# Optimization experiments

Measured on AMD Instinct MI355X. Metric: run time of the kernel, lower is better.

The kernel has to match this reference:

```python
import jax, jax.numpy as jnp
import numpy as np

DIM = 768
HEADS = 8

def setup_inputs() -> dict:
    key = jax.random.key(0)
    k1, k2, k3, k4 = jax.random.split(key, 4)
    x = jax.random.normal(k1, (4, 2048, DIM), dtype=jnp.float32)
    # torch Linear(D, 3D, bias=False): weight [3D, D]; store transposed [D, 3D]
    W_qkv = jax.random.normal(k2, (DIM, 3 * DIM), dtype=jnp.float32) * (DIM ** -0.5)
    W_o = jax.random.normal(k3, (DIM, DIM), dtype=jnp.float32) * (DIM ** -0.5)
    b_o = jax.random.normal(k4, (DIM,), dtype=jnp.float32) * 0.01
    return {"x": x, "W_qkv": W_qkv, "W_o": W_o, "b_o": b_o}

def reference(x, W_qkv, W_o, b_o):
    B, N, D = x.shape
    H = HEADS
    dh = D // H
    scale = dh ** -0.5
    qkv = x @ W_qkv                                   # [B, N, 3D]
    qkv = qkv.reshape(B, N, 3, H, dh)
    qkv = jnp.transpose(qkv, (2, 0, 3, 1, 4))         # [3, B, H, N, dh]
    Q, K, V = qkv[0], qkv[1], qkv[2]
    scores = jnp.einsum('bhqd,bhkd->bhqk', Q, K) * scale  # [B, H, N, N]
    attn = jax.nn.softmax(scores, axis=-1)
    out = jnp.einsum('bhqk,bhkd->bhqd', attn, V)      # [B, H, N, dh]
    # Faithful to original: reshape [B,H,N,dh] -> [B,N,D] WITHOUT head transpose
    out = out.reshape(B, N, D)
    return out @ W_o + b_o
```

## Files before the change

### kernel.cpp

```cpp
#include <hip/hip_runtime.h>

typedef __attribute__((ext_vector_type(8))) short short8;
typedef __attribute__((ext_vector_type(4))) float f32x4;
typedef __attribute__((ext_vector_type(4))) _Float16 half4;
typedef __attribute__((ext_vector_type(8))) _Float16 half8;
typedef __attribute__((ext_vector_type(2))) __fp16 fp16x2;

#define B_SZ 4
#define NSEQ 2048
#define DIM  768
#define NH   8
#define DH   96

__device__ __forceinline__ unsigned short f2bf(float f) {
  unsigned int u = __float_as_uint(f);
  u += 0x7fffu + ((u >> 16) & 1u);
  return (unsigned short)(u >> 16);
}

__device__ __forceinline__ float fexp2(float x) {
#if __has_builtin(__builtin_amdgcn_exp2f)
  return __builtin_amdgcn_exp2f(x);
#else
  return exp2f(x);
#endif
}

__device__ __forceinline__ void glds16(const void* g, void* l) {
  __builtin_amdgcn_global_load_lds((const __attribute__((address_space(1))) void*)g,
                                   (__attribute__((address_space(3))) void*)l, 16, 0, 0);
}

__global__ __launch_bounds__(256) void prep_kernel(
    const float* __restrict__ x, unsigned short* __restrict__ xb,
    const float* __restrict__ Wqkv, unsigned short* __restrict__ wqkvT,
    const float* __restrict__ Wo, unsigned short* __restrict__ woT)
{
  int blk = blockIdx.x;
  if (blk < 6144) {
    int i = blk * 256 + threadIdx.x;
    float4 v = ((const float4*)x)[i];
    ushort4 o;
    o.x = f2bf(v.x); o.y = f2bf(v.y); o.z = f2bf(v.z); o.w = f2bf(v.w);
    ((ushort4*)xb)[i] = o;
    return;
  }
  __shared__ float tile[32][33];
  const float* W; unsigned short* WT; int ncols, bx, by;
  if (blk < 7872) { int r = blk - 6144; W = Wqkv; WT = wqkvT; ncols = 2304; bx = r % 72; by = r / 72; }
  else            { int r = blk - 7872; W = Wo;   WT = woT;   ncols = 768;  bx = r % 24; by = r / 24; }
  int tx = threadIdx.x & 31, ty = threadIdx.x >> 5;
  int c0 = bx * 32, r0 = by * 32;
#pragma unroll
  for (int i = 0; i < 4; i++)
    tile[ty + i * 8][tx] = W[(size_t)(r0 + ty + i * 8) * ncols + c0 + tx];
  __syncthreads();
#pragma unroll
  for (int i = 0; i < 4; i++)
    WT[(size_t)(c0 + ty + i * 8) * 768 + r0 + tx] = f2bf(tile[tx][ty + i * 8]);
}

template <int EPI>
__global__ __launch_bounds__(256) void gemm_bt(
    const unsigned short* __restrict__ A, const unsigned short* __restrict__ Bt,
    unsigned short* __restrict__ qo, unsigned short* __restrict__ ko,
    _Float16* __restrict__ vo, float* __restrict__ fo,
    const float* __restrict__ bias)
{
  __shared__ unsigned short As[128 * 64];
  __shared__ unsigned short Bs[128 * 64];
  const int t = threadIdx.x;
  const int w = t >> 6, lane = t & 63;
  const int l15 = lane & 15, qd = lane >> 4;
  const int rsw = l15 & 7;
  const int m0 = blockIdx.y * 128, n0 = blockIdx.x * 128;
  const int wm = (w >> 1) * 64, wn = (w & 1) * 64;

  int off[2];
#pragma unroll
  for (int j = 0; j < 2; j++) {
    int cl = j * 64 + lane;
    int r16 = cl >> 3, c = cl & 7;
    off[j] = r16 * DIM + ((c ^ (r16 & 7)) * 8);
  }
  const unsigned short* ga = A  + (size_t)(m0 + w * 16) * DIM;
  const unsigned short* gb = Bt + (size_t)(n0 + w * 16) * DIM;

  f32x4 acc[4][4] = {};

  for (int k0 = 0; k0 < DIM; k0 += 64) {
#pragma unroll
    for (int j = 0; j < 2; j++) {
      glds16(ga + k0 + off[j],            &As[w * 1024 + j * 512]);
      glds16(ga + 64 * DIM + k0 + off[j], &As[4096 + w * 1024 + j * 512]);
      glds16(gb + k0 + off[j],            &Bs[w * 1024 + j * 512]);
      glds16(gb + 64 * DIM + k0 + off[j], &Bs[4096 + w * 1024 + j * 512]);
    }
    __syncthreads();
#pragma unroll
    for (int ks = 0; ks < 2; ks++) {
      short8 af[4], bfr[4];
#pragma unroll
      for (int i = 0; i < 4; i++)
        af[i]  = *(const short8*)&As[(wm + i * 16 + l15) * 64 + (((ks * 4 + qd) ^ rsw)) * 8];
#pragma unroll
      for (int i = 0; i < 4; i++)
        bfr[i] = *(const short8*)&Bs[(wn + i * 16 + l15) * 64 + (((ks * 4 + qd) ^ rsw)) * 8];
#pragma unroll
      for (int mi = 0; mi < 4; mi++)
#pragma unroll
        for (int ni = 0; ni < 4; ni++)
          acc[mi][ni] = __builtin_amdgcn_mfma_f32_16x16x32_bf16(af[mi], bfr[ni], acc[mi][ni], 0, 0, 0);
    }
    __syncthreads();
  }

#pragma unroll
  for (int mi = 0; mi < 4; mi++)
#pragma unroll
    for (int ni = 0; ni < 4; ni++) {
      int rowb = m0 + wm + mi * 16 + qd * 4;
      int col  = n0 + wn + ni * 16 + l15;
      if (EPI == 0) {
        int b = rowb >> 11, n = rowb & 2047;
        int s = col / DIM;
        int rem = col - s * DIM;
        int hh = rem / DH;
        int c = rem - hh * DH;
        size_t bh = (size_t)(b * NH + hh);
        if (s == 2) {
          half4 pk;
#pragma unroll
          for (int r = 0; r < 4; r++) pk[r] = (_Float16)acc[mi][ni][r];
          *(half4*)&vo[(bh * DH + c) * NSEQ + n] = pk;
        } else if (s == 0) {
#pragma unroll
          for (int r = 0; r < 4; r++)
            qo[(bh * NSEQ + n + r) * DH + c] = f2bf(acc[mi][ni][r] * 0.1472444679f);
        } else {
#pragma unroll
          for (int r = 0; r < 4; r++)
            ko[(bh * NSEQ + n + r) * DH + c] = f2bf(acc[mi][ni][r]);
        }
      } else {
#pragma unroll
        for (int r = 0; r < 4; r++)
          fo[(size_t)(rowb + r) * DIM + col] = acc[mi][ni][r] + bias[col];
      }
    }
}

__global__ __launch_bounds__(256, 2) void flash_kernel(
    const unsigned short* __restrict__ Qb, const unsigned short* __restrict__ Kb,
    const _Float16* __restrict__ Vtb, unsigned short* __restrict__ Z)
{
  __shared__ unsigned char smem[49152];

  const int t = threadIdx.x, w = t >> 6, lane = t & 63;
  const int l15 = lane & 15, qd = lane >> 4;
  const int swz = (l15 >> 1) & 3;
  const int vswz = l15 & 7;

  const int bid = blockIdx.x;
  const int h  = bid & 7;
  const int qt = (bid >> 3) & 15;
  const int b  = bid >> 7;

  const size_t bh = (size_t)(b * NH + h);
  const unsigned short* Qg = Qb + (bh * NSEQ + (size_t)qt * 128) * DH;
  const unsigned short* Kg = Kb + bh * NSEQ * DH;
  const _Float16*       Vg = Vtb + bh * (size_t)DH * NSEQ;

  int qoff[6];
#pragma unroll
  for (int i = 0; i < 6; i++) {
    int L = i * 256 + t;
    int r = L / 12, c = L - r * 12;
    qoff[i] = r * 96 + ((c ^ ((r >> 1) & 3)) * 8);
  }
  int koff[3];
#pragma unroll
  for (int i = 0; i < 3; i++) {
    int L = w * 192 + i * 64 + lane;
    int r = L / 12, c = L - r * 12;
    int fk = r >> 4, m = r & 15;
    int key = 32 * (fk & 1) + 4 * (fk >> 1) + 8 * (m >> 2) + (m & 3);
    koff[i] = key * 96 + ((c ^ ((r >> 1) & 3)) * 8);
  }
  int voff[3];
#pragma unroll
  for (int i = 0; i < 3; i++) {
    int L = i * 256 + t;
    int r = L >> 3, c = L & 7;
    voff[i] = r * NSEQ + ((c ^ (r & 7)) * 8);
  }

  short8 qa[2][3];
  f32x4 o[2][7] = {};
  const half8 onef = {(_Float16)1.f, (_Float16)1.f, (_Float16)1.f, (_Float16)1.f,
                      (_Float16)1.f, (_Float16)1.f, (_Float16)1.f, (_Float16)1.f};

  auto stK = [&](int j, int bufoff) {
    unsigned short* Kd = (unsigned short*)(smem + bufoff);
    const unsigned short* Kt = Kg + (size_t)j * 64 * DH;
#pragma unroll
    for (int i = 0; i < 3; i++)
      glds16(Kt + koff[i], &Kd[w * 1536 + i * 512]);
  };
  auto stV = [&](int j, int bufoff) {
    _Float16* Vd = (_Float16*)(smem + bufoff + 12288);
    const _Float16* Vt = Vg + j * 64;
#pragma unroll
    for (int i = 0; i < 3; i++)
      glds16(Vt + voff[i], &Vd[(i * 256 + w * 64) * 8]);
  };

#pragma unroll
  for (int i = 0; i < 6; i++)
    glds16(Qg + qoff[i], &((unsigned short*)(smem + 24576))[i * 2048 + w * 512]);
  stK(0, 0);
  stV(0, 0);
  __syncthreads();

  const unsigned short* Qs = (const unsigned short*)(smem + 24576);
#pragma unroll
  for (int fq = 0; fq < 2; fq++)
#pragma unroll
    for (int ks = 0; ks < 3; ks++)
      qa[fq][ks] = *(const short8*)&Qs[(w * 32 + fq * 16 + l15) * 96 + ((ks * 4 + qd) ^ swz) * 8];
  __syncthreads();

  for (int kt = 0; kt < 32; kt++) {
    const int cur = (kt & 1) * 24576;
    const int oth = 24576 - cur;
    const int nkt = (kt < 31) ? kt + 1 : 31;
    const unsigned short* Ks = (const unsigned short*)(smem + cur);
    const _Float16*       Vs = (const _Float16*)(smem + cur + 12288);

    f32x4 s[2][4];
#pragma unroll
    for (int fq = 0; fq < 2; fq++)
#pragma unroll
      for (int fk = 0; fk < 4; fk++) s[fq][fk] = (f32x4){0.f, 0.f, 0.f, 0.f};

    short8 kfa[6];
#pragma unroll
    for (int i = 0; i < 6; i++) {
      int ks = i >> 2, fk = i & 3;
      kfa[i] = *(const short8*)&Ks[(fk * 16 + l15) * 96 + ((ks * 4 + qd) ^ swz) * 8];
    }
    stK(nkt, oth);
    __builtin_amdgcn_s_barrier();
    __builtin_amdgcn_s_setprio(1);
#pragma unroll
    for (int i = 0; i < 6; i++) {
      int ks = i >> 2, fk = i & 3;
      s[0][fk] = __builtin_amdgcn_mfma_f32_16x16x32_bf16(kfa[i], qa[0][ks], s[0][fk], 0, 0, 0);
      s[1][fk] = __builtin_amdgcn_mfma_f32_16x16x32_bf16(kfa[i], qa[1][ks], s[1][fk], 0, 0, 0);
    }
    __builtin_amdgcn_s_setprio(0);
    __builtin_amdgcn_s_barrier();

    short8 kfb[6];
#pragma unroll
    for (int i = 0; i < 6; i++) {
      int k2 = i + 6, ks = k2 >> 2, fk = k2 & 3;
      kfb[i] = *(const short8*)&Ks[(fk * 16 + l15) * 96 + ((ks * 4 + qd) ^ swz) * 8];
    }
    __builtin_amdgcn_s_barrier();
    __builtin_amdgcn_s_setprio(1);
#pragma unroll
    for (int i = 0; i < 6; i++) {
      int k2 = i + 6, ks = k2 >> 2, fk = k2 & 3;
      s[0][fk] = __builtin_amdgcn_mfma_f32_16x16x32_bf16(kfb[i], qa[0][ks], s[0][fk], 0, 0, 0);
      s[1][fk] = __builtin_amdgcn_mfma_f32_16x16x32_bf16(kfb[i], qa[1][ks], s[1][fk], 0, 0, 0);
    }
    __builtin_amdgcn_s_setprio(0);
    asm volatile("s_waitcnt vmcnt(3)" ::: "memory");
    __builtin_amdgcn_s_barrier();

    half4 pf2[2][4];
#pragma unroll
    for (int fq = 0; fq < 2; fq++)
#pragma unroll
      for (int fk = 0; fk < 4; fk++) {
        union { fp16x2 h2[2]; half4 h4; } u;
        u.h2[0] = __builtin_amdgcn_cvt_pkrtz(fexp2(s[fq][fk][0] - 12.f), fexp2(s[fq][fk][1] - 12.f));
        u.h2[1] = __builtin_amdgcn_cvt_pkrtz(fexp2(s[fq][fk][2] - 12.f), fexp2(s[fq][fk][3] - 12.f));
        pf2[fq][fk] = u.h4;
      }

    half8 vfa[6];
#pragma unroll
    for (int fc = 0; fc < 6; fc++)
      vfa[fc] = *(const half8*)&Vs[(fc * 16 + l15) * 64 + ((0 + qd) ^ vswz) * 8];
    stV(nkt, oth);
    __builtin_amdgcn_s_barrier();
    {
      union { half4 h4[2]; half8 h8; } bu0, bu1;
      bu0.h4[0] = pf2[0][0]; bu0.h4[1] = pf2[0][2];
      bu1.h4[0] = pf2[1][0]; bu1.h4[1] = pf2[1][2];
      __builtin_amdgcn_s_setprio(1);
#pragma unroll
      for (int fc = 0; fc < 6; fc++) {
        o[0][fc] = __builtin_amdgcn_mfma_f32_16x16x32_f16(vfa[fc], bu0.h8, o[0][fc], 0, 0, 0);
        o[1][fc] = __builtin_amdgcn_mfma_f32_16x16x32_f16(vfa[fc], bu1.h8, o[1][fc], 0, 0, 0);
      }
      o[0][6] = __builtin_amdgcn_mfma_f32_16x16x32_f16(onef, bu0.h8, o[0][6], 0, 0, 0);
      o[1][6] = __builtin_amdgcn_mfma_f32_16x16x32_f16(onef, bu1.h8, o[1][6], 0, 0, 0);
      __builtin_amdgcn_s_setprio(0);
    }
    __builtin_amdgcn_s_barrier();

    half8 vfb[6];
#pragma unroll
    for (int fc = 0; fc < 6; fc++)
      vfb[fc] = *(const half8*)&Vs[(fc * 16 + l15) * 64 + ((4 + qd) ^ vswz) * 8];
    __builtin_amdgcn_s_barrier();
    {
      union { half4 h4[2]; half8 h8; } bu0, bu1;
      bu0.h4[0] = pf2[0][1]; bu0.h4[1] = pf2[0][3];
      bu1.h4[0] = pf2[1][1]; bu1.h4[1] = pf2[1][3];
      __builtin_amdgcn_s_setprio(1);
#pragma unroll
      for (int fc = 0; fc < 6; fc++) {
        o[0][fc] = __builtin_amdgcn_mfma_f32_16x16x32_f16(vfb[fc], bu0.h8, o[0][fc], 0, 0, 0);
        o[1][fc] = __builtin_amdgcn_mfma_f32_16x16x32_f16(vfb[fc], bu1.h8, o[1][fc], 0, 0, 0);
      }
      o[0][6] = __builtin_amdgcn_mfma_f32_16x16x32_f16(onef, bu0.h8, o[0][6], 0, 0, 0);
      o[1][6] = __builtin_amdgcn_mfma_f32_16x16x32_f16(onef, bu1.h8, o[1][6], 0, 0, 0);
      __builtin_amdgcn_s_setprio(0);
    }
    asm volatile("s_waitcnt vmcnt(3)" ::: "memory");
    __builtin_amdgcn_s_barrier();
  }

#pragma unroll
  for (int fq = 0; fq < 2; fq++) {
    float inv = 1.0f / o[fq][6][0];
    int q = qt * 128 + w * 32 + fq * 16 + l15;
    size_t zbase = ((size_t)b * NSEQ + h * 256 + (q >> 3)) * DIM + (q & 7) * DH;
#pragma unroll
    for (int fc = 0; fc < 6; fc++)
#pragma unroll
      for (int r = 0; r < 4; r += 2) {
        unsigned int pkd = (unsigned int)f2bf(o[fq][fc][r] * inv)
                         | ((unsigned int)f2bf(o[fq][fc][r + 1] * inv) << 16);
        *(unsigned int*)&Z[zbase + fc * 16 + qd * 4 + r] = pkd;
      }
  }
}

extern "C" void kernel_launch(void* const* d_in, const int* in_sizes, int n_in,
                              void* d_out, int out_size, void* d_ws, size_t ws_size,
                              hipStream_t stream)
{
  (void)in_sizes; (void)n_in; (void)out_size; (void)ws_size;
  const float* x    = (const float*)d_in[0];
  const float* Wqkv = (const float*)d_in[1];
  const float* Wo   = (const float*)d_in[2];
  const float* bo   = (const float*)d_in[3];
  float* out = (float*)d_out;

  unsigned short* ws    = (unsigned short*)d_ws;
  unsigned short* xb    = ws;
  unsigned short* wqkvT = xb    + (size_t)8192 * 768;
  unsigned short* woT   = wqkvT + (size_t)2304 * 768;
  unsigned short* Qw    = woT   + (size_t)768 * 768;
  unsigned short* Kw    = Qw    + (size_t)6291456;
  _Float16*       Vw    = (_Float16*)(Kw + (size_t)6291456);
  unsigned short* Zw    = (unsigned short*)(Vw + (size_t)6291456);

  prep_kernel<<<8448, 256, 0, stream>>>(x, xb, Wqkv, wqkvT, Wo, woT);
  gemm_bt<0><<<dim3(18, 64), 256, 0, stream>>>(xb, wqkvT, Qw, Kw, Vw, nullptr, nullptr);
  flash_kernel<<<512, 256, 0, stream>>>(Qw, Kw, Vw, Zw);
  gemm_bt<1><<<dim3(6, 64), 256, 0, stream>>>(Zw, woT, nullptr, nullptr, nullptr, out, bo);
}
```

Baseline: 209.2 us.

## Double-buffer GEMM LDS tiles and remap blocks for XCD-local L2 reuse

The bf16 GEMM now uses two LDS buffers and prefetches the next K tile while computing on the current one, which hides global-to-LDS load latency. Launch becomes a 1D grid whose block index is remapped so that each XCD handles a contiguous band of row tiles, improving L2 reuse of the A rows. The cost is double the LDS footprint per block, which may reduce occupancy.

```diff
diff --git a/kernel.cpp b/kernel.cpp
--- a/kernel.cpp
+++ b/kernel.cpp
@@ -67,13 +67,19 @@
     _Float16* __restrict__ vo, float* __restrict__ fo,
     const float* __restrict__ bias)
 {
-  __shared__ unsigned short As[128 * 64];
-  __shared__ unsigned short Bs[128 * 64];
+  __shared__ unsigned short As[2][128 * 64];
+  __shared__ unsigned short Bs[2][128 * 64];
   const int t = threadIdx.x;
   const int w = t >> 6, lane = t & 63;
   const int l15 = lane & 15, qd = lane >> 4;
   const int rsw = l15 & 7;
-  const int m0 = blockIdx.y * 128, n0 = blockIdx.x * 128;
+
+  const int NX = (EPI == 0) ? 18 : 6;
+  const int bid = blockIdx.x;
+  const int xcd = bid & 7, idx = bid >> 3;
+  const int by = xcd * 8 + idx / NX;
+  const int bx = idx % NX;
+  const int m0 = by * 128, n0 = bx * 128;
   const int wm = (w >> 1) * 64, wn = (w & 1) * 64;
 
   int off[2];
@@ -86,26 +92,37 @@
   const unsigned short* ga = A  + (size_t)(m0 + w * 16) * DIM;
   const unsigned short* gb = Bt + (size_t)(n0 + w * 16) * DIM;
 
+  auto stage = [&](int buf, int k0) {
+    unsigned short* Ad = &As[buf][0];
+    unsigned short* Bd = &Bs[buf][0];
+#pragma unroll
+    for (int j = 0; j < 2; j++) {
+      glds16(ga + k0 + off[j],            &Ad[w * 1024 + j * 512]);
+      glds16(ga + 64 * DIM + k0 + off[j], &Ad[4096 + w * 1024 + j * 512]);
+      glds16(gb + k0 + off[j],            &Bd[w * 1024 + j * 512]);
+      glds16(gb + 64 * DIM + k0 + off[j], &Bd[4096 + w * 1024 + j * 512]);
+    }
+  };
+
   f32x4 acc[4][4] = {};
 
+  stage(0, 0);
+  __syncthreads();
+
   for (int k0 = 0; k0 < DIM; k0 += 64) {
-#pragma unroll
-    for (int j = 0; j < 2; j++) {
-      glds16(ga + k0 + off[j],            &As[w * 1024 + j * 512]);
-      glds16(ga + 64 * DIM + k0 + off[j], &As[4096 + w * 1024 + j * 512]);
-      glds16(gb + k0 + off[j],            &Bs[w * 1024 + j * 512]);
-      glds16(gb + 64 * DIM + k0 + off[j], &Bs[4096 + w * 1024 + j * 512]);
-    }
-    __syncthreads();
+    const int buf = (k0 >> 6) & 1;
+    if (k0 + 64 < DIM) stage(buf ^ 1, k0 + 64);
+    const unsigned short* Ac = &As[buf][0];
+    const unsigned short* Bc = &Bs[buf][0];
 #pragma unroll
     for (int ks = 0; ks < 2; ks++) {
       short8 af[4], bfr[4];
 #pragma unroll
       for (int i = 0; i < 4; i++)
-        af[i]  = *(const short8*)&As[(wm + i * 16 + l15) * 64 + (((ks * 4 + qd) ^ rsw)) * 8];
+        af[i]  = *(const short8*)&Ac[(wm + i * 16 + l15) * 64 + (((ks * 4 + qd) ^ rsw)) * 8];
 #pragma unroll
       for (int i = 0; i < 4; i++)
-        bfr[i] = *(const short8*)&Bs[(wn + i * 16 + l15) * 64 + (((ks * 4 + qd) ^ rsw)) * 8];
+        bfr[i] = *(const short8*)&Bc[(wn + i * 16 + l15) * 64 + (((ks * 4 + qd) ^ rsw)) * 8];
 #pragma unroll
       for (int mi = 0; mi < 4; mi++)
 #pragma unroll
@@ -372,7 +389,7 @@
   unsigned short* Zw    = (unsigned short*)(Vw + (size_t)6291456);
 
   prep_kernel<<<8448, 256, 0, stream>>>(x, xb, Wqkv, wqkvT, Wo, woT);
-  gemm_bt<0><<<dim3(18, 64), 256, 0, stream>>>(xb, wqkvT, Qw, Kw, Vw, nullptr, nullptr);
+  gemm_bt<0><<<1152, 256, 0, stream>>>(xb, wqkvT, Qw, Kw, Vw, nullptr, nullptr);
   flash_kernel<<<512, 256, 0, stream>>>(Qw, Kw, Vw, Zw);
-  gemm_bt<1><<<dim3(6, 64), 256, 0, stream>>>(Zw, woT, nullptr, nullptr, nullptr, out, bo);
-}
+  gemm_bt<1><<<384, 256, 0, stream>>>(Zw, woT, nullptr, nullptr, nullptr, out, bo);
+}
```

Result: slower. 216.4 us (+3.5%).
